# Kernel optimization log

Hardware: AMD Instinct MI355X
Metric: run time of the kernel (lower is better)

The kernel has to match this reference:

```python
import jax, jax.numpy as jnp
import numpy as np

W_CHAMFER = 1.0
W_SMOOTH = 0.5
K_NEIGHBORS = 8


def _pairwise_sqdist(a, b):
    # a: [B,N,3], b: [B,M,3] -> [B,N,M] squared euclidean distances
    a2 = jnp.sum(a * a, axis=-1)  # [B,N]
    b2 = jnp.sum(b * b, axis=-1)  # [B,M]
    ab = jnp.einsum('bnd,bmd->bnm', a, b)  # [B,N,M]
    d2 = a2[:, :, None] + b2[:, None, :] - 2.0 * ab
    return jnp.maximum(d2, 0.0)


def _chamfer(pc1, pc2):
    d = jnp.sqrt(_pairwise_sqdist(pc1, pc2))  # [B,N,M] euclidean (matches torch.norm)
    d1 = jnp.min(d, axis=2)  # [B,N]
    d2 = jnp.min(d, axis=1)  # [B,M]
    return jnp.mean(d1) + jnp.mean(d2)


def _smoothness(pc, flow, k=K_NEIGHBORS):
    d2 = _pairwise_sqdist(pc, pc)  # [B,N,N]
    # k+1 nearest (squared dist preserves ordering); drop self (index 0)
    _, idx = jax.lax.top_k(-d2, k + 1)  # [B,N,k+1]
    idx = idx[:, :, 1:]  # [B,N,k]
    neighbor_flow = jax.vmap(lambda f, i: f[i])(flow, idx)  # [B,N,k,3]
    diff = flow[:, :, None, :] - neighbor_flow
    return jnp.mean(jnp.linalg.norm(diff, axis=-1))


def setup_inputs() -> dict:
    key = jax.random.key(0)
    k1, k2, k3 = jax.random.split(key, 3)
    B, N, M = 2, 8192, 8192
    pc1 = jax.random.normal(k1, (B, N, 3), dtype=jnp.float32)
    pc2 = jax.random.normal(k2, (B, M, 3), dtype=jnp.float32)
    pred_flow = jax.random.normal(k3, (B, N, 3), dtype=jnp.float32) * 0.1
    return {"pc1": pc1, "pc2": pc2, "pred_flow": pred_flow}


def reference(pc1, pc2, pred_flow):
    pc1_warped = pc1 + pred_flow
    l_chamfer = _chamfer(pc1_warped, pc2)
    l_smooth = _smoothness(pc1, pred_flow)
    return W_CHAMFER * l_chamfer + W_SMOOTH * l_smooth
```

## Files before the change

kernel.cpp:

```cpp
#include <hip/hip_runtime.h>

#define N_PTS 8192
#define BATCH 2
#define KNN 8
#define STILE 2048
#define SM_PPW 8
#define SM_PPB 32
#define SM_BLOCKS (BATCH * N_PTS / SM_PPB)
#define CH_ROWS 256
#define CH_BLOCKS (4 * N_PTS / CH_ROWS)

__device__ __forceinline__ void ce(unsigned &x, unsigned &y) {
    unsigned lo = min(x, y), hi = max(x, y); x = lo; y = hi;
}

__device__ __forceinline__ void insert4(unsigned o[4], unsigned key) {
    unsigned n0 = min(o[0], key);
    unsigned n1 = max(o[0], min(o[1], key));
    unsigned n2 = max(o[1], min(o[2], key));
    unsigned n3 = max(o[2], min(o[3], key));
    o[0]=n0; o[1]=n1; o[2]=n2; o[3]=n3;
}

__device__ __forceinline__ void merge_stage8(unsigned m[8], int d) {
    unsigned p[8], c[8];
    #pragma unroll
    for (int k = 0; k < 8; ++k) p[k] = (unsigned)__shfl_xor((int)m[k], d, 64);
    #pragma unroll
    for (int k = 0; k < 8; ++k) c[k] = min(m[k], p[7-k]);
    ce(c[0],c[4]); ce(c[1],c[5]); ce(c[2],c[6]); ce(c[3],c[7]);
    ce(c[0],c[2]); ce(c[1],c[3]); ce(c[4],c[6]); ce(c[5],c[7]);
    ce(c[0],c[1]); ce(c[2],c[3]); ce(c[4],c[5]); ce(c[6],c[7]);
    #pragma unroll
    for (int k = 0; k < 8; ++k) m[k] = c[k];
}

__device__ __forceinline__ void merge64(unsigned m[8]) {
    merge_stage8(m, 1); merge_stage8(m, 2); merge_stage8(m, 4);
    merge_stage8(m, 8); merge_stage8(m, 16); merge_stage8(m, 32);
}

__global__ __launch_bounds__(256, 4) void mega_kernel(
        const float* __restrict__ pc1, const float* __restrict__ pc2,
        const float* __restrict__ flow, float* __restrict__ out) {
    __shared__ float4 sq[STILE];
    __shared__ float psum[4];
    const int tid = threadIdx.x;
    const int bx = blockIdx.x;

    if (bx < SM_BLOCKS) {
        const int b = bx >> 8, sx = bx & 255;
        const int wv = tid >> 6, lane = tid & 63;
        const int i0w = sx * SM_PPB + wv * SM_PPW;
        const float* P = pc1  + (size_t)b * N_PTS * 3;
        const float* F = flow + (size_t)b * N_PTS * 3;

        float mx[8], my[8], mz[8], p2[8], gr[8];
        unsigned thr[8], o[8][4];
        #pragma unroll
        for (int r = 0; r < 8; ++r) {
            int i = i0w + r;
            float px = P[i*3+0], py = P[i*3+1], pz = P[i*3+2];
            mx[r] = -2.0f * px; my[r] = -2.0f * py; mz[r] = -2.0f * pz;
            p2[r] = fmaf(px, px, fmaf(py, py, pz * pz));
            gr[r] = __builtin_inff();
            thr[r] = 0xFFFFFFFFu;
            #pragma unroll
            for (int k = 0; k < 4; ++k) o[r][k] = 0xFFFFFFFFu;
        }

        auto update_thr = [&]() {
            #pragma unroll
            for (int r = 0; r < 8; ++r) {
                unsigned m0 = o[r][0], m1 = o[r][1], m2 = o[r][2], m3 = o[r][3];
                #pragma unroll
                for (int d = 1; d <= 16; d <<= 1) {
                    unsigned q0 = (unsigned)__shfl_xor((int)m0, d, 64);
                    unsigned q1 = (unsigned)__shfl_xor((int)m1, d, 64);
                    unsigned q2 = (unsigned)__shfl_xor((int)m2, d, 64);
                    unsigned q3 = (unsigned)__shfl_xor((int)m3, d, 64);
                    unsigned c0 = min(m0, q3), c1 = min(m1, q2);
                    unsigned c2 = min(m2, q1), c3 = min(m3, q0);
                    ce(c0, c2); ce(c1, c3); ce(c0, c1); ce(c2, c3);
                    m0 = c0; m1 = c1; m2 = c2; m3 = c3;
                }
                unsigned bound = max(m3, (unsigned)__shfl_xor((int)m3, 32, 64));
                thr[r] = min(thr[r], bound);
                float thr_up = __uint_as_float((thr[r] & 0xFFFFE000u) + 0x4000u);
                gr[r] = thr_up - p2[r];
            }
        };

        auto gated_span = [&](int t0, int st0, int st1) {
            #pragma unroll 2
            for (int st = st0; st < st1; ++st) {
                float4 qa = sq[st * 64 + lane];
                int j = t0 + st * 64 + lane;
                float s[8];
                #pragma unroll
                for (int r = 0; r < 8; ++r)
                    s[r] = fmaf(mx[r], qa.x, fmaf(my[r], qa.y, fmaf(mz[r], qa.z, qa.w)));
                #pragma unroll
                for (int r = 0; r < 8; ++r) {
                    if (__any(s[r] <= gr[r])) {
                        float d2 = fmaxf(s[r] + p2[r], 0.0f);
                        unsigned key = (__float_as_uint(d2) & 0xFFFFE000u) | (unsigned)j;
                        key = (j == i0w + r) ? 0xFFFFFFFFu : key;
                        insert4(o[r], key);
                    }
                }
            }
        };

        #pragma unroll 1
        for (int tile = 0; tile < N_PTS / STILE; ++tile) {
            const int t0 = tile * STILE;
            __syncthreads();
            #pragma unroll
            for (int u = tid; u < STILE; u += 256) {
                int g = t0 + u;
                float qx = P[g*3+0], qy = P[g*3+1], qz = P[g*3+2];
                sq[u] = make_float4(qx, qy, qz, fmaf(qx, qx, fmaf(qy, qy, qz * qz)));
            }
            __syncthreads();

            if (tile == 0) {
                #pragma unroll 4
                for (int st = 0; st < 16; ++st) {
                    float4 qa = sq[st * 64 + lane];
                    int j = st * 64 + lane;
                    #pragma unroll
                    for (int r = 0; r < 8; ++r) {
                        float ss = fmaf(mx[r], qa.x, fmaf(my[r], qa.y, fmaf(mz[r], qa.z, qa.w)));
                        float d2 = fmaxf(ss + p2[r], 0.0f);
                        unsigned key = (__float_as_uint(d2) & 0xFFFFE000u) | (unsigned)j;
                        key = (j == i0w + r) ? 0xFFFFFFFFu : key;
                        insert4(o[r], key);
                    }
                }
                update_thr();
                gated_span(0, 16, 32);
            } else {
                gated_span(t0, 0, 32);
                if (tile == 1) update_thr();
            }
        }

        const int pr = lane >> 3, kk = lane & 7;
        unsigned mykey = 0xFFFFFFFFu;
        #pragma unroll
        for (int r = 0; r < 8; ++r) {
            unsigned m[8] = {o[r][0], o[r][1], o[r][2], o[r][3],
                             0xFFFFFFFFu, 0xFFFFFFFFu, 0xFFFFFFFFu, 0xFFFFFFFFu};
            merge64(m);
            if (pr == r) {
                unsigned k2 = m[0];
                #pragma unroll
                for (int t = 1; t < 8; ++t) k2 = (kk == t) ? m[t] : k2;
                mykey = k2;
            }
        }
        const int i = i0w + pr;
        const int j = (int)(mykey & (N_PTS - 1));
        float dx = F[i*3+0] - F[j*3+0];
        float dy = F[i*3+1] - F[j*3+1];
        float dz = F[i*3+2] - F[j*3+2];
        float sv = sqrtf(fmaf(dx, dx, fmaf(dy, dy, dz * dz)));
        #pragma unroll
        for (int d = 1; d < 64; d <<= 1) sv += __shfl_xor(sv, d, 64);
        if (lane == 0) psum[wv] = sv;
        __syncthreads();
        if (tid == 0) {
            atomicAdd(out, (psum[0] + psum[1] + psum[2] + psum[3]) *
                           (0.5f / ((float)BATCH * N_PTS * KNN)));
        }
    } else {
        const int cb = bx - SM_BLOCKS;
        const int z  = cb >> 5;
        const int rb = cb & 31;
        const int b = z & 1, dir = z >> 1;
        const float* P1 = pc1  + (size_t)b * N_PTS * 3;
        const float* P2 = pc2  + (size_t)b * N_PTS * 3;
        const float* FL = flow + (size_t)b * N_PTS * 3;
        const int wv = tid >> 6, lane = tid & 63;
        const int rw = tid >> 1, sub = tid & 1;
        const int r0 = rb * CH_ROWS + rw * 2;

        float mx0, my0, mz0, p20, mx1, my1, mz1, p21;
        {
            float px, py, pz;
            if (dir == 0) {
                px = P1[r0*3+0] + FL[r0*3+0];
                py = P1[r0*3+1] + FL[r0*3+1];
                pz = P1[r0*3+2] + FL[r0*3+2];
            } else {
                px = P2[r0*3+0]; py = P2[r0*3+1]; pz = P2[r0*3+2];
            }
            mx0 = -2.0f * px; my0 = -2.0f * py; mz0 = -2.0f * pz;
            p20 = fmaf(px, px, fmaf(py, py, pz * pz));
            int r1 = r0 + 1;
            if (dir == 0) {
                px = P1[r1*3+0] + FL[r1*3+0];
                py = P1[r1*3+1] + FL[r1*3+1];
                pz = P1[r1*3+2] + FL[r1*3+2];
            } else {
                px = P2[r1*3+0]; py = P2[r1*3+1]; pz = P2[r1*3+2];
            }
            mx1 = -2.0f * px; my1 = -2.0f * py; mz1 = -2.0f * pz;
            p21 = fmaf(px, px, fmaf(py, py, pz * pz));
        }
        float b0 = __builtin_inff(), b1 = __builtin_inff();

        #pragma unroll 1
        for (int tile = 0; tile < N_PTS / STILE; ++tile) {
            const int t0 = tile * STILE;
            __syncthreads();
            #pragma unroll
            for (int u = tid; u < STILE; u += 256) {
                int g = t0 + u;
                float qx, qy, qz;
                if (dir == 0) {
                    qx = P2[g*3+0]; qy = P2[g*3+1]; qz = P2[g*3+2];
                } else {
                    qx = P1[g*3+0] + FL[g*3+0];
                    qy = P1[g*3+1] + FL[g*3+1];
                    qz = P1[g*3+2] + FL[g*3+2];
                }
                sq[u] = make_float4(qx, qy, qz, fmaf(qx, qx, fmaf(qy, qy, qz * qz)));
            }
            __syncthreads();

            const float4* base = sq + sub * (STILE / 2);
            #pragma unroll 8
            for (int c = 0; c < STILE / 2; ++c) {
                float4 q = base[c];
                float s0 = fmaf(mx0, q.x, fmaf(my0, q.y, fmaf(mz0, q.z, q.w)));
                float s1 = fmaf(mx1, q.x, fmaf(my1, q.y, fmaf(mz1, q.z, q.w)));
                b0 = fminf(b0, s0);
                b1 = fminf(b1, s1);
            }
        }

        b0 = fminf(b0, __shfl_xor(b0, 1, 64));
        b1 = fminf(b1, __shfl_xor(b1, 1, 64));
        float val = (sub == 0)
            ? (sqrtf(fmaxf(b0 + p20, 0.0f)) + sqrtf(fmaxf(b1 + p21, 0.0f)))
            : 0.0f;
        #pragma unroll
        for (int d = 1; d < 64; d <<= 1) val += __shfl_xor(val, d, 64);
        if (lane == 0) psum[wv] = val;
        __syncthreads();
        if (tid == 0) {
            atomicAdd(out, (psum[0] + psum[1] + psum[2] + psum[3]) *
                           (1.0f / ((float)BATCH * N_PTS)));
        }
    }
}

extern "C" void kernel_launch(void* const* d_in, const int* in_sizes, int n_in,
                              void* d_out, int out_size, void* d_ws, size_t ws_size,
                              hipStream_t stream) {
    const float* pc1  = (const float*)d_in[0];
    const float* pc2  = (const float*)d_in[1];
    const float* flow = (const float*)d_in[2];
    float* out = (float*)d_out;

    hipMemsetAsync(out, 0, sizeof(float), stream);
    mega_kernel<<<dim3(SM_BLOCKS + CH_BLOCKS), 256, 0, stream>>>(pc1, pc2, flow, out);
}
```

Baseline: 165.7 us.

## Rebalance work split, reorder chamfer blocks first, replace atomics with finish kernel

Smoothness blocks now handle 4 query points per wave instead of 8, which doubles the number of kNN blocks. Chamfer blocks shrink to 64 rows with 8 threads splitting the candidates, and they are scheduled before the kNN blocks. The pruning threshold is refreshed more often during the later tiles. Per-block partial sums go to a workspace and a single-block finish kernel reduces them, replacing the memset and atomics. The cost is a second kernel launch and more redundant LDS tile loading across blocks.

Measured after the change: 138.3 us. -16.5%, faster.

```diff
diff --git a/kernel.cpp b/kernel.cpp
--- a/kernel.cpp
+++ b/kernel.cpp
@@ -4,11 +4,11 @@
 #define BATCH 2
 #define KNN 8
 #define STILE 2048
-#define SM_PPW 8
-#define SM_PPB 32
+#define SM_PPB 16
 #define SM_BLOCKS (BATCH * N_PTS / SM_PPB)
-#define CH_ROWS 256
-#define CH_BLOCKS (4 * N_PTS / CH_ROWS)
+#define CH_BLOCKS 512
+#define NBLOCKS (CH_BLOCKS + SM_BLOCKS)
+#define OFF_SMSUM 512
 
 __device__ __forceinline__ void ce(unsigned &x, unsigned &y) {
     unsigned lo = min(x, y), hi = max(x, y); x = lo; y = hi;
@@ -42,23 +42,104 @@
 
 __global__ __launch_bounds__(256, 4) void mega_kernel(
         const float* __restrict__ pc1, const float* __restrict__ pc2,
-        const float* __restrict__ flow, float* __restrict__ out) {
+        const float* __restrict__ flow, float* __restrict__ chsum,
+        float* __restrict__ smsum) {
     __shared__ float4 sq[STILE];
     __shared__ float psum[4];
     const int tid = threadIdx.x;
     const int bx = blockIdx.x;
 
-    if (bx < SM_BLOCKS) {
-        const int b = bx >> 8, sx = bx & 255;
+    if (bx < CH_BLOCKS) {
+        const int z  = bx >> 7;
+        const int rb = bx & 127;
+        const int b = z & 1, dir = z >> 1;
+        const float* P1 = pc1  + (size_t)b * N_PTS * 3;
+        const float* P2 = pc2  + (size_t)b * N_PTS * 3;
+        const float* FL = flow + (size_t)b * N_PTS * 3;
         const int wv = tid >> 6, lane = tid & 63;
-        const int i0w = sx * SM_PPB + wv * SM_PPW;
+        const int sub = tid & 7;
+        const int r0 = rb * 64 + 2 * (tid >> 3);
+
+        float mx0, my0, mz0, p20, mx1, my1, mz1, p21;
+        {
+            float px, py, pz;
+            if (dir == 0) {
+                px = P1[r0*3+0] + FL[r0*3+0];
+                py = P1[r0*3+1] + FL[r0*3+1];
+                pz = P1[r0*3+2] + FL[r0*3+2];
+            } else {
+                px = P2[r0*3+0]; py = P2[r0*3+1]; pz = P2[r0*3+2];
+            }
+            mx0 = -2.0f * px; my0 = -2.0f * py; mz0 = -2.0f * pz;
+            p20 = fmaf(px, px, fmaf(py, py, pz * pz));
+            int r1 = r0 + 1;
+            if (dir == 0) {
+                px = P1[r1*3+0] + FL[r1*3+0];
+                py = P1[r1*3+1] + FL[r1*3+1];
+                pz = P1[r1*3+2] + FL[r1*3+2];
+            } else {
+                px = P2[r1*3+0]; py = P2[r1*3+1]; pz = P2[r1*3+2];
+            }
+            mx1 = -2.0f * px; my1 = -2.0f * py; mz1 = -2.0f * pz;
+            p21 = fmaf(px, px, fmaf(py, py, pz * pz));
+        }
+        float b0 = __builtin_inff(), b1 = __builtin_inff();
+
+        #pragma unroll 1
+        for (int tile = 0; tile < N_PTS / STILE; ++tile) {
+            const int t0 = tile * STILE;
+            __syncthreads();
+            #pragma unroll
+            for (int u = tid; u < STILE; u += 256) {
+                int g = t0 + u;
+                float qx, qy, qz;
+                if (dir == 0) {
+                    qx = P2[g*3+0]; qy = P2[g*3+1]; qz = P2[g*3+2];
+                } else {
+                    qx = P1[g*3+0] + FL[g*3+0];
+                    qy = P1[g*3+1] + FL[g*3+1];
+                    qz = P1[g*3+2] + FL[g*3+2];
+                }
+                sq[u] = make_float4(qx, qy, qz, fmaf(qx, qx, fmaf(qy, qy, qz * qz)));
+            }
+            __syncthreads();
+
+            #pragma unroll 8
+            for (int c = 0; c < STILE / 8; ++c) {
+                float4 q = sq[c * 8 + sub];
+                float s0 = fmaf(mx0, q.x, fmaf(my0, q.y, fmaf(mz0, q.z, q.w)));
+                float s1 = fmaf(mx1, q.x, fmaf(my1, q.y, fmaf(mz1, q.z, q.w)));
+                b0 = fminf(b0, s0);
+                b1 = fminf(b1, s1);
+            }
+        }
+
+        #pragma unroll
+        for (int d = 1; d <= 4; d <<= 1) {
+            b0 = fminf(b0, __shfl_xor(b0, d, 64));
+            b1 = fminf(b1, __shfl_xor(b1, d, 64));
+        }
+        float val = (sub == 0)
+            ? (sqrtf(fmaxf(b0 + p20, 0.0f)) + sqrtf(fmaxf(b1 + p21, 0.0f)))
+            : 0.0f;
+        #pragma unroll
+        for (int d = 1; d < 64; d <<= 1) val += __shfl_xor(val, d, 64);
+        if (lane == 0) psum[wv] = val;
+        __syncthreads();
+        if (tid == 0) chsum[bx] = psum[0] + psum[1] + psum[2] + psum[3];
+    } else {
+        const int s  = bx - CH_BLOCKS;
+        const int b  = s >> 9;
+        const int sx = s & 511;
+        const int wv = tid >> 6, lane = tid & 63;
+        const int i0w = sx * SM_PPB + wv * 4;
         const float* P = pc1  + (size_t)b * N_PTS * 3;
         const float* F = flow + (size_t)b * N_PTS * 3;
 
-        float mx[8], my[8], mz[8], p2[8], gr[8];
-        unsigned thr[8], o[8][4];
-        #pragma unroll
-        for (int r = 0; r < 8; ++r) {
+        float mx[4], my[4], mz[4], p2[4], gr[4];
+        unsigned thr[4], o[4][4];
+        #pragma unroll
+        for (int r = 0; r < 4; ++r) {
             int i = i0w + r;
             float px = P[i*3+0], py = P[i*3+1], pz = P[i*3+2];
             mx[r] = -2.0f * px; my[r] = -2.0f * py; mz[r] = -2.0f * pz;
@@ -71,7 +152,7 @@
 
         auto update_thr = [&]() {
             #pragma unroll
-            for (int r = 0; r < 8; ++r) {
+            for (int r = 0; r < 4; ++r) {
                 unsigned m0 = o[r][0], m1 = o[r][1], m2 = o[r][2], m3 = o[r][3];
                 #pragma unroll
                 for (int d = 1; d <= 16; d <<= 1) {
@@ -96,14 +177,14 @@
             for (int st = st0; st < st1; ++st) {
                 float4 qa = sq[st * 64 + lane];
                 int j = t0 + st * 64 + lane;
-                float s[8];
+                float sc[4];
                 #pragma unroll
-                for (int r = 0; r < 8; ++r)
-                    s[r] = fmaf(mx[r], qa.x, fmaf(my[r], qa.y, fmaf(mz[r], qa.z, qa.w)));
+                for (int r = 0; r < 4; ++r)
+                    sc[r] = fmaf(mx[r], qa.x, fmaf(my[r], qa.y, fmaf(mz[r], qa.z, qa.w)));
                 #pragma unroll
-                for (int r = 0; r < 8; ++r) {
-                    if (__any(s[r] <= gr[r])) {
-                        float d2 = fmaxf(s[r] + p2[r], 0.0f);
+                for (int r = 0; r < 4; ++r) {
+                    if (__any(sc[r] <= gr[r])) {
+                        float d2 = fmaxf(sc[r] + p2[r], 0.0f);
                         unsigned key = (__float_as_uint(d2) & 0xFFFFE000u) | (unsigned)j;
                         key = (j == i0w + r) ? 0xFFFFFFFFu : key;
                         insert4(o[r], key);
@@ -130,7 +211,7 @@
                     float4 qa = sq[st * 64 + lane];
                     int j = st * 64 + lane;
                     #pragma unroll
-                    for (int r = 0; r < 8; ++r) {
+                    for (int r = 0; r < 4; ++r) {
                         float ss = fmaf(mx[r], qa.x, fmaf(my[r], qa.y, fmaf(mz[r], qa.z, qa.w)));
                         float d2 = fmaxf(ss + p2[r], 0.0f);
                         unsigned key = (__float_as_uint(d2) & 0xFFFFE000u) | (unsigned)j;
@@ -140,28 +221,32 @@
                 }
                 update_thr();
                 gated_span(0, 16, 32);
+                update_thr();
             } else {
                 gated_span(t0, 0, 32);
-                if (tile == 1) update_thr();
-            }
-        }
-
-        const int pr = lane >> 3, kk = lane & 7;
-        unsigned mykey = 0xFFFFFFFFu;
-        #pragma unroll
-        for (int r = 0; r < 8; ++r) {
+                if (tile <= 2) update_thr();
+            }
+        }
+
+        unsigned fin[4][8];
+        #pragma unroll
+        for (int r = 0; r < 4; ++r) {
             unsigned m[8] = {o[r][0], o[r][1], o[r][2], o[r][3],
                              0xFFFFFFFFu, 0xFFFFFFFFu, 0xFFFFFFFFu, 0xFFFFFFFFu};
             merge64(m);
-            if (pr == r) {
-                unsigned k2 = m[0];
-                #pragma unroll
-                for (int t = 1; t < 8; ++t) k2 = (kk == t) ? m[t] : k2;
-                mykey = k2;
-            }
-        }
-        const int i = i0w + pr;
-        const int j = (int)(mykey & (N_PTS - 1));
+            #pragma unroll
+            for (int k = 0; k < 8; ++k) fin[r][k] = m[k];
+        }
+        const int sel = lane & 31;
+        unsigned key = fin[0][0];
+        #pragma unroll
+        for (int rr = 0; rr < 4; ++rr)
+            #pragma unroll
+            for (int kk = 0; kk < 8; ++kk)
+                if (sel == rr * 8 + kk) key = fin[rr][kk];
+        const int r = sel >> 3;
+        const int i = i0w + r;
+        const int j = (int)(key & (N_PTS - 1));
         float dx = F[i*3+0] - F[j*3+0];
         float dy = F[i*3+1] - F[j*3+1];
         float dz = F[i*3+2] - F[j*3+2];
@@ -170,90 +255,29 @@
         for (int d = 1; d < 64; d <<= 1) sv += __shfl_xor(sv, d, 64);
         if (lane == 0) psum[wv] = sv;
         __syncthreads();
-        if (tid == 0) {
-            atomicAdd(out, (psum[0] + psum[1] + psum[2] + psum[3]) *
-                           (0.5f / ((float)BATCH * N_PTS * KNN)));
-        }
-    } else {
-        const int cb = bx - SM_BLOCKS;
-        const int z  = cb >> 5;
-        const int rb = cb & 31;
-        const int b = z & 1, dir = z >> 1;
-        const float* P1 = pc1  + (size_t)b * N_PTS * 3;
-        const float* P2 = pc2  + (size_t)b * N_PTS * 3;
-        const float* FL = flow + (size_t)b * N_PTS * 3;
-        const int wv = tid >> 6, lane = tid & 63;
-        const int rw = tid >> 1, sub = tid & 1;
-        const int r0 = rb * CH_ROWS + rw * 2;
-
-        float mx0, my0, mz0, p20, mx1, my1, mz1, p21;
-        {
-            float px, py, pz;
-            if (dir == 0) {
-                px = P1[r0*3+0] + FL[r0*3+0];
-                py = P1[r0*3+1] + FL[r0*3+1];
-                pz = P1[r0*3+2] + FL[r0*3+2];
-            } else {
-                px = P2[r0*3+0]; py = P2[r0*3+1]; pz = P2[r0*3+2];
-            }
-            mx0 = -2.0f * px; my0 = -2.0f * py; mz0 = -2.0f * pz;
-            p20 = fmaf(px, px, fmaf(py, py, pz * pz));
-            int r1 = r0 + 1;
-            if (dir == 0) {
-                px = P1[r1*3+0] + FL[r1*3+0];
-                py = P1[r1*3+1] + FL[r1*3+1];
-                pz = P1[r1*3+2] + FL[r1*3+2];
-            } else {
-                px = P2[r1*3+0]; py = P2[r1*3+1]; pz = P2[r1*3+2];
-            }
-            mx1 = -2.0f * px; my1 = -2.0f * py; mz1 = -2.0f * pz;
-            p21 = fmaf(px, px, fmaf(py, py, pz * pz));
-        }
-        float b0 = __builtin_inff(), b1 = __builtin_inff();
-
-        #pragma unroll 1
-        for (int tile = 0; tile < N_PTS / STILE; ++tile) {
-            const int t0 = tile * STILE;
-            __syncthreads();
-            #pragma unroll
-            for (int u = tid; u < STILE; u += 256) {
-                int g = t0 + u;
-                float qx, qy, qz;
-                if (dir == 0) {
-                    qx = P2[g*3+0]; qy = P2[g*3+1]; qz = P2[g*3+2];
-                } else {
-                    qx = P1[g*3+0] + FL[g*3+0];
-                    qy = P1[g*3+1] + FL[g*3+1];
-                    qz = P1[g*3+2] + FL[g*3+2];
-                }
-                sq[u] = make_float4(qx, qy, qz, fmaf(qx, qx, fmaf(qy, qy, qz * qz)));
-            }
-            __syncthreads();
-
-            const float4* base = sq + sub * (STILE / 2);
-            #pragma unroll 8
-            for (int c = 0; c < STILE / 2; ++c) {
-                float4 q = base[c];
-                float s0 = fmaf(mx0, q.x, fmaf(my0, q.y, fmaf(mz0, q.z, q.w)));
-                float s1 = fmaf(mx1, q.x, fmaf(my1, q.y, fmaf(mz1, q.z, q.w)));
-                b0 = fminf(b0, s0);
-                b1 = fminf(b1, s1);
-            }
-        }
-
-        b0 = fminf(b0, __shfl_xor(b0, 1, 64));
-        b1 = fminf(b1, __shfl_xor(b1, 1, 64));
-        float val = (sub == 0)
-            ? (sqrtf(fmaxf(b0 + p20, 0.0f)) + sqrtf(fmaxf(b1 + p21, 0.0f)))
-            : 0.0f;
-        #pragma unroll
-        for (int d = 1; d < 64; d <<= 1) val += __shfl_xor(val, d, 64);
-        if (lane == 0) psum[wv] = val;
-        __syncthreads();
-        if (tid == 0) {
-            atomicAdd(out, (psum[0] + psum[1] + psum[2] + psum[3]) *
-                           (1.0f / ((float)BATCH * N_PTS)));
-        }
+        if (tid == 0)
+            smsum[s] = psum[0] + psum[1] + psum[2] + psum[3];
+    }
+}
+
+__global__ __launch_bounds__(512) void finish_kernel(const float* __restrict__ chsum,
+                                                     const float* __restrict__ smsum,
+                                                     float* __restrict__ out) {
+    const int t = threadIdx.x;
+    float ch = chsum[t];
+    float sm = smsum[t] + smsum[t + 512];
+    float local = ch * (1.0f / (float)(BATCH * N_PTS))
+                + sm * (0.25f / ((float)BATCH * N_PTS * KNN));
+    #pragma unroll
+    for (int d = 1; d < 64; d <<= 1) local += __shfl_xor(local, d, 64);
+    __shared__ float wsum[8];
+    if ((t & 63) == 0) wsum[t >> 6] = local;
+    __syncthreads();
+    if (t == 0) {
+        float tot = 0.0f;
+        #pragma unroll
+        for (int k = 0; k < 8; ++k) tot += wsum[k];
+        out[0] = tot;
     }
 }
 
@@ -264,7 +288,9 @@
     const float* pc2  = (const float*)d_in[1];
     const float* flow = (const float*)d_in[2];
     float* out = (float*)d_out;
-
-    hipMemsetAsync(out, 0, sizeof(float), stream);
-    mega_kernel<<<dim3(SM_BLOCKS + CH_BLOCKS), 256, 0, stream>>>(pc1, pc2, flow, out);
-}
+    float* chsum = (float*)d_ws;
+    float* smsum = (float*)d_ws + OFF_SMSUM;
+
+    mega_kernel<<<dim3(NBLOCKS), 256, 0, stream>>>(pc1, pc2, flow, chsum, smsum);
+    finish_kernel<<<dim3(1), 512, 0, stream>>>(chsum, smsum, out);
+}
```
